# Kernel optimization log

Hardware: AMD Instinct MI355X
Metric: run time of the kernel (lower is better)

The kernel has to match this reference:

```python
import jax, jax.numpy as jnp
import numpy as np

B, T, D, H = 2, 2048, 1024, 16
DH = D // H
THETA = 10000.0
MAX_SEQ_LEN = 2048


def setup_inputs() -> dict:
    key = jax.random.key(0)
    kx, kqkv, ko = jax.random.split(key, 3)
    # trunc_normal init matching the torch Linear (std=sqrt(2/(fan_in+fan_out)), clipped at 3 sigma)
    sigma_qkv = (2.0 / (D + 3 * D)) ** 0.5
    sigma_o = (2.0 / (D + D)) ** 0.5
    W_qkv = jax.random.truncated_normal(kqkv, -3.0, 3.0, (3 * D, D), jnp.float32) * sigma_qkv
    W_o = jax.random.truncated_normal(ko, -3.0, 3.0, (D, D), jnp.float32) * sigma_o
    # RoPE caches: angles[t, i] = t / theta^(2i/d_k)
    dims = jnp.arange(0, DH, 2, dtype=jnp.float32)
    inv_freq = 1.0 / (THETA ** (dims / DH))  # [DH/2]
    angles = jnp.arange(MAX_SEQ_LEN, dtype=jnp.float32)[:, None] * inv_freq[None, :]  # [T, DH/2]
    return {
        "x": jax.random.normal(kx, (B, T, D), jnp.float32),
        "token_positions": jnp.arange(T, dtype=jnp.int64 if jax.config.jax_enable_x64 else jnp.int32),
        "W_qkv": W_qkv,
        "W_o": W_o,
        "cos_cached": jnp.cos(angles),
        "sin_cached": jnp.sin(angles),
    }


def _apply_rope(x, cos, sin):
    # x: [b, h, t, dh]; cos/sin: [t, dh/2] broadcast over (b, h)
    x1 = x[..., 0::2]
    x2 = x[..., 1::2]
    r1 = x1 * cos - x2 * sin
    r2 = x1 * sin + x2 * cos
    # interleave back: (.., dh/2, 2) -> (.., dh)
    return jnp.stack([r1, r2], axis=-1).reshape(x.shape)


def reference(x, token_positions, W_qkv, W_o, cos_cached, sin_cached):
    b, t, d = x.shape
    qkv = jnp.einsum("btd,ed->bte", x, W_qkv)  # [b, t, 3d]
    q, k, v = jnp.split(qkv, 3, axis=-1)

    def to_heads(z):
        return z.reshape(b, t, H, DH).transpose(0, 2, 1, 3)  # [b, h, t, dh]

    q, k, v = to_heads(q), to_heads(k), to_heads(v)

    cos = cos_cached[token_positions]  # [t, dh/2]
    sin = sin_cached[token_positions]
    q = _apply_rope(q, cos, sin)
    k = _apply_rope(k, cos, sin)

    scale = 1.0 / jnp.sqrt(jnp.asarray(DH, x.dtype))
    scores = jnp.einsum("bhqd,bhkd->bhqk", q, k) * scale  # full TxT (naive, matches source)
    causal = jnp.tril(jnp.ones((t, t), dtype=bool))  # [t, t]
    scores = jnp.where(causal[None, None, :, :], scores, -jnp.inf)
    attn = jax.nn.softmax(scores, axis=-1)
    out = jnp.einsum("bhqk,bhkd->bhqd", attn, v)  # [b, h, t, dh]
    out = out.transpose(0, 2, 1, 3).reshape(b, t, d)
    return jnp.einsum("btd,ed->bte", out, W_o)
```

## Files before the change

kernel.cpp:

```cpp
#include <hip/hip_runtime.h>
#include <hip/hip_bf16.h>
#include <stdint.h>

#define Bn  2
#define Tn  2048
#define Dn  1024
#define Hn  16
#define DHn 64
#define QSCALE 0.1803368801111204f

typedef unsigned short u16;
typedef __attribute__((ext_vector_type(8))) short s16x8;
typedef __attribute__((ext_vector_type(8))) unsigned short u16x8;
typedef __attribute__((ext_vector_type(4))) unsigned short u16x4;
typedef __attribute__((ext_vector_type(4))) float f32x4;

#define MFMA(a, b, c) __builtin_amdgcn_mfma_f32_16x16x32_bf16((a), (b), (c), 0, 0, 0)

__device__ __forceinline__ u16 f2bf(float f) {
  union { __hip_bfloat16 b; u16 u; } c;
  c.b = __float2bfloat16(f);
  return c.u;
}
__device__ __forceinline__ float bf2f(u16 u) {
  union { u16 u; __hip_bfloat16 b; } c;
  c.u = u;
  return __bfloat162float(c.b);
}

__device__ __forceinline__ void lds16(void* lds, const void* g) {
  __builtin_amdgcn_global_load_lds((__attribute__((address_space(1))) void*)(g),
                                   (__attribute__((address_space(3))) void*)(lds), 16, 0, 0);
}

__global__ __launch_bounds__(256) void k_cvt(const float* __restrict__ src,
                                             u16* __restrict__ dst, int n4) {
  int i = blockIdx.x * blockDim.x + threadIdx.x;
  const int stride = gridDim.x * blockDim.x;
  for (; i < n4; i += stride) {
    float4 v = ((const float4*)src)[i];
    u16x4 o;
    o[0] = f2bf(v.x); o[1] = f2bf(v.y); o[2] = f2bf(v.z); o[3] = f2bf(v.w);
    ((u16x4*)dst)[i] = o;
  }
}

__global__ __launch_bounds__(256) void k_qkv(
    const u16* __restrict__ xb, const u16* __restrict__ wb,
    const int* __restrict__ tokpos,
    const float* __restrict__ cosc, const float* __restrict__ sinc,
    u16* __restrict__ qb, u16* __restrict__ kb, u16* __restrict__ vtb)
{
  __shared__ u16 smem[17408];
  u16* As = smem;
  u16* Bs = smem + 8192;
  const int tid  = threadIdx.x;
  const int bcol = blockIdx.x;
  const int brow = blockIdx.y;
  const int lane = tid & 63, w = tid >> 6;
  const int wr = w >> 1, wc = w & 1;
  const int l15 = lane & 15, l4 = lane >> 4;
  const int lrow = lane >> 3;
  const int gsw  = ((lane & 7) ^ (lane >> 3)) * 8;
  const int rsw  = l15 & 7;

  f32x4 acc[4][4] = {};

  for (int k0 = 0; k0 < 1024; k0 += 64) {
#pragma unroll
    for (int c = 0; c < 4; ++c) {
      const int r0 = w * 32 + c * 8;
      lds16(&As[r0 * 64], xb + (size_t)(brow * 128 + r0 + lrow) * 1024 + k0 + gsw);
      lds16(&Bs[r0 * 64], wb + (size_t)(bcol * 128 + r0 + lrow) * 1024 + k0 + gsw);
    }
    __syncthreads();
#pragma unroll
    for (int kk = 0; kk < 64; kk += 32) {
      const int gc = (kk >> 3) + l4;
      s16x8 af[4], bf[4];
#pragma unroll
      for (int m = 0; m < 4; ++m)
        af[m] = *(const s16x8*)&As[(wr * 64 + m * 16 + l15) * 64 + ((gc ^ rsw) * 8)];
#pragma unroll
      for (int n = 0; n < 4; ++n)
        bf[n] = *(const s16x8*)&Bs[(wc * 64 + n * 16 + l15) * 64 + ((gc ^ rsw) * 8)];
#pragma unroll
      for (int m = 0; m < 4; ++m)
#pragma unroll
        for (int n = 0; n < 4; ++n)
          acc[m][n] = MFMA(af[m], bf[n], acc[m][n]);
    }
    __syncthreads();
  }

#pragma unroll
  for (int m = 0; m < 4; ++m)
#pragma unroll
    for (int n = 0; n < 4; ++n)
#pragma unroll
      for (int r = 0; r < 4; ++r)
        smem[(wr * 64 + m * 16 + l4 * 4 + r) * 136 + wc * 64 + n * 16 + l15] =
            f2bf(acc[m][n][r]);
  __syncthreads();

  if (bcol < 16) {
    u16* dst; float sc;
    if (bcol < 8) { dst = qb; sc = QSCALE; } else { dst = kb; sc = 1.0f; }
#pragma unroll
    for (int ph = 0; ph < 8; ++ph) {
      const int task = ph * 256 + tid;
      const int lr   = task >> 4;
      const int cg   = task & 15;
      const int rowg = brow * 128 + lr;
      const int b = rowg >> 11, t = rowg & 2047;
      const int rem = (bcol * 128 + cg * 8) & 1023;
      const int h = rem >> 6, dh0 = rem & 63;
      u16x8 v = *(const u16x8*)&smem[lr * 136 + cg * 8];
      const int pos = tokpos[t];
      const float4 cv = *(const float4*)&cosc[pos * 32 + (dh0 >> 1)];
      const float4 sv = *(const float4*)&sinc[pos * 32 + (dh0 >> 1)];
      const float cc[4] = {cv.x, cv.y, cv.z, cv.w};
      const float ss[4] = {sv.x, sv.y, sv.z, sv.w};
      u16x8 o;
#pragma unroll
      for (int p = 0; p < 4; ++p) {
        const float x1 = bf2f(v[2 * p]), x2 = bf2f(v[2 * p + 1]);
        o[2 * p]     = f2bf((x1 * cc[p] - x2 * ss[p]) * sc);
        o[2 * p + 1] = f2bf((x1 * ss[p] + x2 * cc[p]) * sc);
      }
      *(u16x8*)(dst + ((size_t)(b * Hn + h) * Tn + t) * DHn + dh0) = o;
    }
  } else {
    const int b  = (brow * 128) >> 11;
    const int t0 = (brow * 128) & 2047;
#pragma unroll
    for (int ph = 0; ph < 8; ++ph) {
      const int task = ph * 256 + tid;
      const int col = task & 127;
      const int tg  = task >> 7;
      const int h  = 2 * (bcol - 16) + (col >> 6);
      const int dh = col & 63;
      u16x8 v;
#pragma unroll
      for (int j = 0; j < 8; ++j) v[j] = smem[(tg * 8 + j) * 136 + col];
      *(u16x8*)(vtb + ((size_t)(b * Hn + h) * DHn + dh) * Tn + t0 + tg * 8) = v;
    }
  }
}

__global__ __launch_bounds__(256) void k_attn(
    const u16* __restrict__ qbuf, const u16* __restrict__ kbuf,
    const u16* __restrict__ vtb, u16* __restrict__ ob)
{
  __shared__ u16 Ks[2][64][64];
  __shared__ u16 Vs[2][64][64];
  __shared__ u16 Ps[4][16][64];

  const int tid  = threadIdx.x;
  const int lane = tid & 63, w = tid >> 6;
  const int l15 = lane & 15, l4 = lane >> 4;
  const int lrow = lane >> 3;
  const int gsw  = ((lane & 7) ^ (lane >> 3)) * 8;
  const int rsw  = l15 & 7;

  const int lin = blockIdx.x;
  const int xcd = lin & 7, i = lin >> 3;
  const int c = i & 31, r = i >> 5;
  const int bh   = xcd + 8 * r;
  const int qblk = (r & 1) ? (31 - c) : c;
  const int b = bh >> 4, h = bh & 15;

  const u16* Qh = qbuf + (size_t)bh * Tn * DHn;
  const u16* Kh = kbuf + (size_t)bh * Tn * DHn;
  const u16* Vh = vtb  + (size_t)bh * DHn * Tn;

  const int q0 = qblk * 64 + w * 16;
  const int ntiles = qblk + 1;

  const s16x8 qf0 = *(const s16x8*)(Qh + (size_t)(q0 + l15) * 64 + l4 * 8);
  const s16x8 qf1 = *(const s16x8*)(Qh + (size_t)(q0 + l15) * 64 + 32 + l4 * 8);

  const s16x8 onesv = {(short)0x3F80, (short)0x3F80, (short)0x3F80, (short)0x3F80,
                       (short)0x3F80, (short)0x3F80, (short)0x3F80, (short)0x3F80};

  f32x4 o[4] = {};
  f32x4 o5 = {};
  float m = -3.0e38f;

  {
    const int r0 = w * 16;
    lds16(&Ks[0][r0][0],     Kh + (size_t)(r0 + lrow) * 64 + gsw);
    lds16(&Ks[0][r0 + 8][0], Kh + (size_t)(r0 + 8 + lrow) * 64 + gsw);
    lds16(&Vs[0][r0][0],     Vh + (size_t)(r0 + lrow) * Tn + gsw);
    lds16(&Vs[0][r0 + 8][0], Vh + (size_t)(r0 + 8 + lrow) * Tn + gsw);
  }

  for (int it = 0; it < ntiles; ++it) {
    const int buf = it & 1;
    __syncthreads();
    if (it + 1 < ntiles) {
      const int nb = buf ^ 1;
      const int kv1 = (it + 1) * 64;
      const int r0 = w * 16;
      lds16(&Ks[nb][r0][0],     Kh + (size_t)(kv1 + r0 + lrow) * 64 + gsw);
      lds16(&Ks[nb][r0 + 8][0], Kh + (size_t)(kv1 + r0 + 8 + lrow) * 64 + gsw);
      lds16(&Vs[nb][r0][0],     Vh + (size_t)(r0 + lrow) * Tn + kv1 + gsw);
      lds16(&Vs[nb][r0 + 8][0], Vh + (size_t)(r0 + 8 + lrow) * Tn + kv1 + gsw);
    }

    f32x4 s[4] = {};
    __builtin_amdgcn_s_setprio(1);
#pragma unroll
    for (int ks = 0; ks < 2; ++ks) {
      const s16x8 qf = ks ? qf1 : qf0;
      const int gr = ((ks * 4 + l4) ^ rsw) * 8;
#pragma unroll
      for (int hh = 0; hh < 4; ++hh) {
        const s16x8 kf = *(const s16x8*)&Ks[buf][hh * 16 + l15][gr];
        s[hh] = MFMA(kf, qf, s[hh]);
      }
    }
    __builtin_amdgcn_s_setprio(0);

    if (it == ntiles - 1) {
      const int kvb = it * 64 + l4 * 4;
      const int qg  = q0 + l15;
#pragma unroll
      for (int hh = 0; hh < 4; ++hh)
#pragma unroll
        for (int rr = 0; rr < 4; ++rr)
          if (kvb + hh * 16 + rr > qg) s[hh][rr] = -3.0e38f;
    }

    const float a0 = fmaxf(fmaxf(s[0][0], s[0][1]), s[0][2]);
    const float a1 = fmaxf(fmaxf(s[0][3], s[1][0]), s[1][1]);
    const float a2 = fmaxf(fmaxf(s[1][2], s[1][3]), s[2][0]);
    const float a3 = fmaxf(fmaxf(s[2][1], s[2][2]), s[2][3]);
    const float a4 = fmaxf(fmaxf(s[3][0], s[3][1]), s[3][2]);
    float tmax = fmaxf(fmaxf(fmaxf(a0, a1), fmaxf(a2, a3)), fmaxf(a4, s[3][3]));
    tmax = fmaxf(tmax, __shfl_xor(tmax, 16));
    tmax = fmaxf(tmax, __shfl_xor(tmax, 32));

    if (__any(tmax > m + 8.0f)) {
      const float mn    = fmaxf(m, tmax);
      const float alpha = __builtin_amdgcn_exp2f(m - mn);
      m = mn;
#pragma unroll
      for (int n = 0; n < 4; ++n)
#pragma unroll
        for (int rr = 0; rr < 4; ++rr) o[n][rr] *= alpha;
#pragma unroll
      for (int rr = 0; rr < 4; ++rr) o5[rr] *= alpha;
    }

#pragma unroll
    for (int hh = 0; hh < 4; ++hh) {
      u16x4 pk;
#pragma unroll
      for (int rr = 0; rr < 4; ++rr)
        pk[rr] = f2bf(__builtin_amdgcn_exp2f(s[hh][rr] - m));
      const int pg = ((hh << 1) + (l4 >> 1)) ^ rsw;
      *(u16x4*)&Ps[w][l15][pg * 8 + (l4 & 1) * 4] = pk;
    }

    const s16x8 pf0 = *(const s16x8*)&Ps[w][l15][(l4 ^ rsw) * 8];
    const s16x8 pf1 = *(const s16x8*)&Ps[w][l15][((4 + l4) ^ rsw) * 8];

    __builtin_amdgcn_s_setprio(1);
#pragma unroll
    for (int n = 0; n < 4; ++n) {
      const int g0 = (l4 ^ rsw) * 8, g1 = ((4 + l4) ^ rsw) * 8;
      const s16x8 vf0 = *(const s16x8*)&Vs[buf][n * 16 + l15][g0];
      const s16x8 vf1 = *(const s16x8*)&Vs[buf][n * 16 + l15][g1];
      o[n] = MFMA(vf0, pf0, o[n]);
      o[n] = MFMA(vf1, pf1, o[n]);
    }
    o5 = MFMA(onesv, pf0, o5);
    o5 = MFMA(onesv, pf1, o5);
    __builtin_amdgcn_s_setprio(0);
  }

  const float inv = 1.0f / o5[0];
  const int t = q0 + l15;
#pragma unroll
  for (int n = 0; n < 4; ++n) {
    u16x4 ov;
#pragma unroll
    for (int rr = 0; rr < 4; ++rr) ov[rr] = f2bf(o[n][rr] * inv);
    *(u16x4*)(ob + (size_t)(b * Tn + t) * Dn + h * 64 + n * 16 + l4 * 4) = ov;
  }
}

__global__ __launch_bounds__(256) void k_out(
    const u16* __restrict__ ob, const u16* __restrict__ wob,
    float* __restrict__ out)
{
  __shared__ u16 smem[8192];
  u16* As = smem;
  u16* Bs = smem + 4096;
  const int tid  = threadIdx.x;
  const int bcol = blockIdx.x;
  const int brow = blockIdx.y;
  const int lane = tid & 63, w = tid >> 6;
  const int wr = w >> 1, wc = w & 1;
  const int l15 = lane & 15, l4 = lane >> 4;
  const int lrow = lane >> 3;
  const int gsw  = ((lane & 7) ^ (lane >> 3)) * 8;
  const int rsw  = l15 & 7;

  f32x4 acc[2][2] = {};

  for (int k0 = 0; k0 < 1024; k0 += 64) {
#pragma unroll
    for (int cc = 0; cc < 2; ++cc) {
      const int r0 = w * 16 + cc * 8;
      lds16(&As[r0 * 64], ob  + (size_t)(brow * 64 + r0 + lrow) * 1024 + k0 + gsw);
      lds16(&Bs[r0 * 64], wob + (size_t)(bcol * 64 + r0 + lrow) * 1024 + k0 + gsw);
    }
    __syncthreads();
#pragma unroll
    for (int kk = 0; kk < 64; kk += 32) {
      const int gc = (kk >> 3) + l4;
      s16x8 af[2], bf[2];
#pragma unroll
      for (int mm = 0; mm < 2; ++mm)
        af[mm] = *(const s16x8*)&As[(wr * 32 + mm * 16 + l15) * 64 + ((gc ^ rsw) * 8)];
#pragma unroll
      for (int n = 0; n < 2; ++n)
        bf[n] = *(const s16x8*)&Bs[(wc * 32 + n * 16 + l15) * 64 + ((gc ^ rsw) * 8)];
#pragma unroll
      for (int mm = 0; mm < 2; ++mm)
#pragma unroll
        for (int n = 0; n < 2; ++n)
          acc[mm][n] = MFMA(af[mm], bf[n], acc[mm][n]);
    }
    __syncthreads();
  }

#pragma unroll
  for (int mm = 0; mm < 2; ++mm) {
    const int rowb = brow * 64 + wr * 32 + mm * 16 + l4 * 4;
#pragma unroll
    for (int n = 0; n < 2; ++n) {
      const int colg = bcol * 64 + wc * 32 + n * 16 + l15;
#pragma unroll
      for (int rr = 0; rr < 4; ++rr)
        out[(size_t)(rowb + rr) * 1024 + colg] = acc[mm][n][rr];
    }
  }
}

extern "C" void kernel_launch(void* const* d_in, const int* in_sizes, int n_in,
                              void* d_out, int out_size, void* d_ws, size_t ws_size,
                              hipStream_t stream) {
  const float* x      = (const float*)d_in[0];
  const int*   tokpos = (const int*)d_in[1];
  const float* wqkv   = (const float*)d_in[2];
  const float* wo     = (const float*)d_in[3];
  const float* cosc   = (const float*)d_in[4];
  const float* sinc   = (const float*)d_in[5];
  float* out = (float*)d_out;

  u16* xb    = (u16*)d_ws;
  u16* wqkvb = xb + (size_t)Bn * Tn * Dn;
  u16* qb    = wqkvb + (size_t)3 * Dn * Dn;
  u16* kb    = qb + (size_t)Bn * Tn * Dn;
  u16* vtb   = kb + (size_t)Bn * Tn * Dn;
  u16* ob    = xb;
  u16* wob   = wqkvb;

  dim3 blk(256);
  k_cvt<<<dim3(2048), blk, 0, stream>>>(x,    xb,    (Bn * Tn * Dn) / 4);
  k_cvt<<<dim3(2048), blk, 0, stream>>>(wqkv, wqkvb, (3 * Dn * Dn) / 4);

  k_qkv<<<dim3(24, 32), blk, 0, stream>>>(xb, wqkvb, tokpos, cosc, sinc, qb, kb, vtb);

  k_cvt<<<dim3(1024), blk, 0, stream>>>(wo, wob, (Dn * Dn) / 4);

  k_attn<<<dim3(1024), blk, 0, stream>>>(qb, kb, vtb, ob);

  k_out<<<dim3(16, 64), blk, 0, stream>>>(ob, wob, out);
}
```

Before: 119.6 us.

## Double-buffer GEMM K-loops, retile output projection, fuse conversions, remap attention blocks

Double-buffers the LDS K-tiles in the QKV and output-projection GEMMs, using explicit vmcnt waits and raw barriers so the next tile's global-to-LDS loads overlap the current tile's MFMAs. The attention loop swaps __syncthreads for the same waitcnt plus barrier pattern, and its block mapping now issues the heaviest (largest causal) query blocks first. The output GEMM tile grows to 128x64 for more reuse per block. The x and W_qkv bf16 conversions are merged into one launch. The larger LDS footprint may lower occupancy, and the new attention mapping drops the XCD-aware placement.

After: 107.9 us. 9.7% less time.

```diff
diff --git a/kernel.cpp b/kernel.cpp
--- a/kernel.cpp
+++ b/kernel.cpp
@@ -31,6 +31,20 @@
 __device__ __forceinline__ void lds16(void* lds, const void* g) {
   __builtin_amdgcn_global_load_lds((__attribute__((address_space(1))) void*)(g),
                                    (__attribute__((address_space(3))) void*)(lds), 16, 0, 0);
+}
+
+__global__ __launch_bounds__(256) void k_cvt2(const float* __restrict__ s0, int n0,
+                                              const float* __restrict__ s1, int n1,
+                                              u16* __restrict__ dst) {
+  int i = blockIdx.x * blockDim.x + threadIdx.x;
+  const int stride = gridDim.x * blockDim.x;
+  const int nt = n0 + n1;
+  for (; i < nt; i += stride) {
+    float4 v = (i < n0) ? ((const float4*)s0)[i] : ((const float4*)s1)[i - n0];
+    u16x4 o;
+    o[0] = f2bf(v.x); o[1] = f2bf(v.y); o[2] = f2bf(v.z); o[3] = f2bf(v.w);
+    ((u16x4*)dst)[i] = o;
+  }
 }
 
 __global__ __launch_bounds__(256) void k_cvt(const float* __restrict__ src,
@@ -51,9 +65,7 @@
     const float* __restrict__ cosc, const float* __restrict__ sinc,
     u16* __restrict__ qb, u16* __restrict__ kb, u16* __restrict__ vtb)
 {
-  __shared__ u16 smem[17408];
-  u16* As = smem;
-  u16* Bs = smem + 8192;
+  __shared__ u16 smem[32768];
   const int tid  = threadIdx.x;
   const int bcol = blockIdx.x;
   const int brow = blockIdx.y;
@@ -66,31 +78,53 @@
 
   f32x4 acc[4][4] = {};
 
-  for (int k0 = 0; k0 < 1024; k0 += 64) {
-#pragma unroll
-    for (int c = 0; c < 4; ++c) {
-      const int r0 = w * 32 + c * 8;
-      lds16(&As[r0 * 64], xb + (size_t)(brow * 128 + r0 + lrow) * 1024 + k0 + gsw);
-      lds16(&Bs[r0 * 64], wb + (size_t)(bcol * 128 + r0 + lrow) * 1024 + k0 + gsw);
-    }
-    __syncthreads();
+#pragma unroll
+  for (int c = 0; c < 4; ++c) {
+    const int r0 = w * 32 + c * 8;
+    lds16(&smem[r0 * 64],         xb + (size_t)(brow * 128 + r0 + lrow) * 1024 + gsw);
+    lds16(&smem[16384 + r0 * 64], wb + (size_t)(bcol * 128 + r0 + lrow) * 1024 + gsw);
+  }
+
+  for (int kt = 0; kt < 16; ++kt) {
+    const int cur = kt & 1;
+    const u16* Asb = smem + cur * 8192;
+    const u16* Bsb = smem + 16384 + cur * 8192;
+    if (kt < 15) {
+      u16* Asn = smem + (cur ^ 1) * 8192;
+      u16* Bsn = smem + 16384 + (cur ^ 1) * 8192;
+      const int k1 = (kt + 1) * 64;
+#pragma unroll
+      for (int c = 0; c < 4; ++c) {
+        const int r0 = w * 32 + c * 8;
+        lds16(&Asn[r0 * 64], xb + (size_t)(brow * 128 + r0 + lrow) * 1024 + k1 + gsw);
+        lds16(&Bsn[r0 * 64], wb + (size_t)(bcol * 128 + r0 + lrow) * 1024 + k1 + gsw);
+      }
+      asm volatile("s_waitcnt vmcnt(8)" ::: "memory");
+    } else {
+      asm volatile("s_waitcnt vmcnt(0)" ::: "memory");
+    }
+    __builtin_amdgcn_s_barrier();
+    __builtin_amdgcn_sched_barrier(0);
+    __builtin_amdgcn_s_setprio(1);
 #pragma unroll
     for (int kk = 0; kk < 64; kk += 32) {
       const int gc = (kk >> 3) + l4;
       s16x8 af[4], bf[4];
 #pragma unroll
       for (int m = 0; m < 4; ++m)
-        af[m] = *(const s16x8*)&As[(wr * 64 + m * 16 + l15) * 64 + ((gc ^ rsw) * 8)];
+        af[m] = *(const s16x8*)&Asb[(wr * 64 + m * 16 + l15) * 64 + ((gc ^ rsw) * 8)];
 #pragma unroll
       for (int n = 0; n < 4; ++n)
-        bf[n] = *(const s16x8*)&Bs[(wc * 64 + n * 16 + l15) * 64 + ((gc ^ rsw) * 8)];
+        bf[n] = *(const s16x8*)&Bsb[(wc * 64 + n * 16 + l15) * 64 + ((gc ^ rsw) * 8)];
 #pragma unroll
       for (int m = 0; m < 4; ++m)
 #pragma unroll
         for (int n = 0; n < 4; ++n)
           acc[m][n] = MFMA(af[m], bf[n], acc[m][n]);
     }
-    __syncthreads();
+    __builtin_amdgcn_s_setprio(0);
+    __builtin_amdgcn_sched_barrier(0);
+    __builtin_amdgcn_s_barrier();
   }
 
 #pragma unroll
@@ -163,11 +197,9 @@
   const int gsw  = ((lane & 7) ^ (lane >> 3)) * 8;
   const int rsw  = l15 & 7;
 
-  const int lin = blockIdx.x;
-  const int xcd = lin & 7, i = lin >> 3;
-  const int c = i & 31, r = i >> 5;
-  const int bh   = xcd + 8 * r;
-  const int qblk = (r & 1) ? (31 - c) : c;
+  const int lin  = blockIdx.x;
+  const int bh   = lin & 31;
+  const int qblk = 31 - (lin >> 5);
   const int b = bh >> 4, h = bh & 15;
 
   const u16* Qh = qbuf + (size_t)bh * Tn * DHn;
@@ -197,7 +229,6 @@
 
   for (int it = 0; it < ntiles; ++it) {
     const int buf = it & 1;
-    __syncthreads();
     if (it + 1 < ntiles) {
       const int nb = buf ^ 1;
       const int kv1 = (it + 1) * 64;
@@ -206,7 +237,12 @@
       lds16(&Ks[nb][r0 + 8][0], Kh + (size_t)(kv1 + r0 + 8 + lrow) * 64 + gsw);
       lds16(&Vs[nb][r0][0],     Vh + (size_t)(r0 + lrow) * Tn + kv1 + gsw);
       lds16(&Vs[nb][r0 + 8][0], Vh + (size_t)(r0 + 8 + lrow) * Tn + kv1 + gsw);
-    }
+      asm volatile("s_waitcnt vmcnt(4)" ::: "memory");
+    } else {
+      asm volatile("s_waitcnt vmcnt(0)" ::: "memory");
+    }
+    __builtin_amdgcn_s_barrier();
+    __builtin_amdgcn_sched_barrier(0);
 
     f32x4 s[4] = {};
     __builtin_amdgcn_s_setprio(1);
@@ -278,6 +314,8 @@
     o5 = MFMA(onesv, pf0, o5);
     o5 = MFMA(onesv, pf1, o5);
     __builtin_amdgcn_s_setprio(0);
+    __builtin_amdgcn_sched_barrier(0);
+    __builtin_amdgcn_s_barrier();
   }
 
   const float inv = 1.0f / o5[0];
@@ -295,9 +333,7 @@
     const u16* __restrict__ ob, const u16* __restrict__ wob,
     float* __restrict__ out)
 {
-  __shared__ u16 smem[8192];
-  u16* As = smem;
-  u16* Bs = smem + 4096;
+  __shared__ u16 smem[24576];
   const int tid  = threadIdx.x;
   const int bcol = blockIdx.x;
   const int brow = blockIdx.y;
@@ -308,44 +344,74 @@
   const int gsw  = ((lane & 7) ^ (lane >> 3)) * 8;
   const int rsw  = l15 & 7;
 
-  f32x4 acc[2][2] = {};
-
-  for (int k0 = 0; k0 < 1024; k0 += 64) {
-#pragma unroll
-    for (int cc = 0; cc < 2; ++cc) {
-      const int r0 = w * 16 + cc * 8;
-      lds16(&As[r0 * 64], ob  + (size_t)(brow * 64 + r0 + lrow) * 1024 + k0 + gsw);
-      lds16(&Bs[r0 * 64], wob + (size_t)(bcol * 64 + r0 + lrow) * 1024 + k0 + gsw);
-    }
-    __syncthreads();
+  f32x4 acc[4][2] = {};
+
+#pragma unroll
+  for (int c = 0; c < 4; ++c) {
+    const int r0 = w * 32 + c * 8;
+    lds16(&smem[r0 * 64], ob + (size_t)(brow * 128 + r0 + lrow) * 1024 + gsw);
+  }
+#pragma unroll
+  for (int c = 0; c < 2; ++c) {
+    const int r0 = w * 16 + c * 8;
+    lds16(&smem[16384 + r0 * 64], wob + (size_t)(bcol * 64 + r0 + lrow) * 1024 + gsw);
+  }
+
+  for (int kt = 0; kt < 16; ++kt) {
+    const int cur = kt & 1;
+    const u16* Asb = smem + cur * 8192;
+    const u16* Bsb = smem + 16384 + cur * 4096;
+    if (kt < 15) {
+      u16* Asn = smem + (cur ^ 1) * 8192;
+      u16* Bsn = smem + 16384 + (cur ^ 1) * 4096;
+      const int k1 = (kt + 1) * 64;
+#pragma unroll
+      for (int c = 0; c < 4; ++c) {
+        const int r0 = w * 32 + c * 8;
+        lds16(&Asn[r0 * 64], ob + (size_t)(brow * 128 + r0 + lrow) * 1024 + k1 + gsw);
+      }
+#pragma unroll
+      for (int c = 0; c < 2; ++c) {
+        const int r0 = w * 16 + c * 8;
+        lds16(&Bsn[r0 * 64], wob + (size_t)(bcol * 64 + r0 + lrow) * 1024 + k1 + gsw);
+      }
+      asm volatile("s_waitcnt vmcnt(6)" ::: "memory");
+    } else {
+      asm volatile("s_waitcnt vmcnt(0)" ::: "memory");
+    }
+    __builtin_amdgcn_s_barrier();
+    __builtin_amdgcn_sched_barrier(0);
+    __builtin_amdgcn_s_setprio(1);
 #pragma unroll
     for (int kk = 0; kk < 64; kk += 32) {
       const int gc = (kk >> 3) + l4;
-      s16x8 af[2], bf[2];
-#pragma unroll
-      for (int mm = 0; mm < 2; ++mm)
-        af[mm] = *(const s16x8*)&As[(wr * 32 + mm * 16 + l15) * 64 + ((gc ^ rsw) * 8)];
+      s16x8 af[4], bf[2];
+#pragma unroll
+      for (int m = 0; m < 4; ++m)
+        af[m] = *(const s16x8*)&Asb[(wr * 64 + m * 16 + l15) * 64 + ((gc ^ rsw) * 8)];
 #pragma unroll
       for (int n = 0; n < 2; ++n)
-        bf[n] = *(const s16x8*)&Bs[(wc * 32 + n * 16 + l15) * 64 + ((gc ^ rsw) * 8)];
-#pragma unroll
-      for (int mm = 0; mm < 2; ++mm)
+        bf[n] = *(const s16x8*)&Bsb[(wc * 32 + n * 16 + l15) * 64 + ((gc ^ rsw) * 8)];
+#pragma unroll
+      for (int m = 0; m < 4; ++m)
 #pragma unroll
         for (int n = 0; n < 2; ++n)
-          acc[mm][n] = MFMA(af[mm], bf[n], acc[mm][n]);
-    }
-    __syncthreads();
-  }
-
-#pragma unroll
-  for (int mm = 0; mm < 2; ++mm) {
-    const int rowb = brow * 64 + wr * 32 + mm * 16 + l4 * 4;
+          acc[m][n] = MFMA(af[m], bf[n], acc[m][n]);
+    }
+    __builtin_amdgcn_s_setprio(0);
+    __builtin_amdgcn_sched_barrier(0);
+    __builtin_amdgcn_s_barrier();
+  }
+
+#pragma unroll
+  for (int m = 0; m < 4; ++m) {
+    const int rowb = brow * 128 + wr * 64 + m * 16 + l4 * 4;
 #pragma unroll
     for (int n = 0; n < 2; ++n) {
       const int colg = bcol * 64 + wc * 32 + n * 16 + l15;
 #pragma unroll
-      for (int rr = 0; rr < 4; ++rr)
-        out[(size_t)(rowb + rr) * 1024 + colg] = acc[mm][n][rr];
+      for (int r = 0; r < 4; ++r)
+        out[(size_t)(rowb + r) * 1024 + colg] = acc[m][n][r];
     }
   }
 }
@@ -370,8 +436,8 @@
   u16* wob   = wqkvb;
 
   dim3 blk(256);
-  k_cvt<<<dim3(2048), blk, 0, stream>>>(x,    xb,    (Bn * Tn * Dn) / 4);
-  k_cvt<<<dim3(2048), blk, 0, stream>>>(wqkv, wqkvb, (3 * Dn * Dn) / 4);
+  k_cvt2<<<dim3(2048), blk, 0, stream>>>(x, (Bn * Tn * Dn) / 4,
+                                         wqkv, (3 * Dn * Dn) / 4, xb);
 
   k_qkv<<<dim3(24, 32), blk, 0, stream>>>(xb, wqkvb, tokpos, cosc, sinc, qb, kb, vtb);
 
@@ -379,5 +445,5 @@
 
   k_attn<<<dim3(1024), blk, 0, stream>>>(qb, kb, vtb, ob);
 
-  k_out<<<dim3(16, 64), blk, 0, stream>>>(ob, wob, out);
-}
+  k_out<<<dim3(16, 32), blk, 0, stream>>>(ob, wob, out);
+}
```
